# Optimization experiments

Hardware: AMD Instinct MI355X
Metric: run time of the kernel (lower is better)

Reference implementation:

```python
import jax, jax.numpy as jnp
import numpy as np

A, B, D, H = 64, 256, 128, 512  # seq rows, columns (encoder batch / decode loop), n_dims, hidden


def _lstm_step(Wih, Whh, bih, bhh, h, c, x):
    # x: [N, D], h/c: [N, H]; PyTorch gate order i, f, g, o
    gates = x @ Wih.T + bih + h @ Whh.T + bhh  # [N, 4H]
    i, f, g, o = jnp.split(gates, 4, axis=-1)
    c = jax.nn.sigmoid(f) * c + jax.nn.sigmoid(i) * jnp.tanh(g)
    h = jax.nn.sigmoid(o) * jnp.tanh(c)
    return h, c


def setup_inputs() -> dict:
    key = jax.random.key(0)
    ks = jax.random.split(key, 12)
    s = 0.05
    inp = {
        "input_tensor": jax.random.normal(ks[0], (A, B, D), jnp.float32),
        "enc_Wih": jax.random.normal(ks[1], (4 * H, D), jnp.float32) * s,
        "enc_Whh": jax.random.normal(ks[2], (4 * H, H), jnp.float32) * s,
        "enc_bih": jax.random.normal(ks[3], (4 * H,), jnp.float32) * s,
        "enc_bhh": jax.random.normal(ks[4], (4 * H,), jnp.float32) * s,
        "dec_Wih": jax.random.normal(ks[5], (4 * H, D), jnp.float32) * s,
        "dec_Whh": jax.random.normal(ks[6], (4 * H, H), jnp.float32) * s,
        "dec_bih": jax.random.normal(ks[7], (4 * H,), jnp.float32) * s,
        "dec_bhh": jax.random.normal(ks[8], (4 * H,), jnp.float32) * s,
        "lin_W": jax.random.normal(ks[9], (D, H), jnp.float32) * s,
        "lin_b": jax.random.normal(ks[10], (D,), jnp.float32) * s,
    }
    return inp


def reference(input_tensor, enc_Wih, enc_Whh, enc_bih, enc_bhh,
              dec_Wih, dec_Whh, dec_bih, dec_bhh, lin_W, lin_b):
    a, b, d = input_tensor.shape
    h_dim = enc_Whh.shape[1]
    dt = input_tensor.dtype

    # ---- encoder: seq-first LSTM over dim0 (len a), batch = b ----
    def e_step(hc, x_t):
        h, c = hc
        h, c = _lstm_step(enc_Wih, enc_Whh, enc_bih, enc_bhh, h, c, x_t)
        return (h, c), None

    h0 = jnp.zeros((b, h_dim), dt)
    (hN, cN), _ = jax.lax.scan(e_step, (h0, h0), input_tensor)
    # hidden[0][:, -1].unsqueeze(1): keep only the LAST batch element -> [1, H]
    dh, dc = hN[-1:], cN[-1:]

    # ---- decoder: loop i = b-1 .. 0; emit linear(h) then run length-a LSTM on column i ----
    def col_step(hc, x_col):  # x_col: [a, d]
        h, c = hc
        out_i = (h @ lin_W.T + lin_b)[0]  # [d], emitted BEFORE processing the column

        def t_step(hc2, x_t):
            h2, c2 = hc2
            h2, c2 = _lstm_step(dec_Wih, dec_Whh, dec_bih, dec_bhh, h2, c2, x_t[None])
            return (h2, c2), None

        (h, c), _ = jax.lax.scan(t_step, (h, c), x_col)
        return (h, c), out_i

    x_cols = jnp.flip(jnp.transpose(input_tensor, (1, 0, 2)), 0)  # [b, a, d], reversed i
    _, outs = jax.lax.scan(col_step, (dh, dc), x_cols)  # [b, d] in reversed order
    outs = jnp.flip(outs, 0)
    # outputs[:, i, :] = [1, d] row broadcast across all a rows
    return jnp.broadcast_to(outs[None, :, :], (a, b, d))
```

## Files before the change

### kernel.cpp

```cpp
#include <hip/hip_runtime.h>
#include <math.h>

#define A_ 64
#define B_ 256
#define D_ 128
#define H_ 512
#define STEPS_ENC 64
#define STEPS_TOT (64 + 16384)
#define NWG 32

#define XCC_GETREG_IMM (20 | (31 << 11))

#define OFF_XT    0
#define N_XT      (A_*D_*B_)
#define OFF_HT0   (OFF_XT + N_XT)
#define OFF_HT1   (OFF_HT0 + H_*B_)
#define OFF_CT    (OFF_HT1 + H_*B_)
#define OFF_HTAP  (OFF_CT + H_*B_)
#define OFF_HB64  (OFF_HTAP + B_*H_)
#define OFF_CINIT (OFF_HB64 + 4*H_)
#define OFF_ELECT (OFF_CINIT + H_)

__device__ __forceinline__ float tanhfast(float x) {
  return 1.0f - 2.0f * __builtin_amdgcn_rcpf(__expf(2.0f * x) + 1.0f);
}

__device__ __forceinline__ unsigned long long load_nt(const unsigned long long* p) {
  unsigned long long v;
  asm volatile("global_load_dwordx2 %0, %1, off nt\n\ts_waitcnt vmcnt(0)"
               : "=&v"(v) : "v"(p) : "memory");
  return v;
}
__device__ __forceinline__ unsigned long long load_inv(const unsigned long long* p) {
  unsigned long long v;
  asm volatile("buffer_inv sc0\n\t"
               "global_load_dwordx2 %0, %1, off nt\n\ts_waitcnt vmcnt(0)"
               : "=&v"(v) : "v"(p) : "memory");
  return v;
}
__device__ __forceinline__ void store_nt(unsigned long long* p, unsigned long long v) {
  asm volatile("global_store_dwordx2 %0, %1, off nt" :: "v"(p), "v"(v) : "memory");
}

template<int CTRL>
__device__ __forceinline__ float dpp_ror_add(float x) {
  int y = __builtin_amdgcn_update_dpp(0, __float_as_int(x), CTRL, 0xF, 0xF, false);
  return x + __int_as_float(y);
}
__device__ __forceinline__ float row_allsum16(float x) {
  x = dpp_ror_add<0x128>(x);
  x = dpp_ror_add<0x124>(x);
  x = dpp_ror_add<0x122>(x);
  x = dpp_ror_add<0x121>(x);
  return x;
}

#define HSP 36
#define HS_N (16 * HSP)

__global__ void init0(float* __restrict__ ws) {
  unsigned long long* HB = (unsigned long long*)(ws + OFF_HB64);
  int* EL = (int*)(ws + OFF_ELECT);
  int j = threadIdx.x;
  HB[H_ + j] = 0ull;
  HB[j]      = 0xFFFFFFFF00000000ull;
  if (j < 8) EL[j] = 0;
  if (j == 8) EL[8] = -1;
}

template<int PHASE>
__device__ __forceinline__ void lstm_phase(
    const float* __restrict__ in0,
    const float* __restrict__ Wih, const float* __restrict__ Whh,
    const float* __restrict__ bih, const float* __restrict__ bhh,
    unsigned long long* __restrict__ HB, float* __restrict__ HTAP,
    float* hstage,
    int w, int v, int l, float& c,
    float actA, float actB, float actC)
{
  const int g = l >> 4;
  const int j = l & 15;
  const int u = (w << 4) + v;
  const int R = (g << 9) + u;

  float4 wh[8];
#pragma unroll
  for (int k = 0; k < 8; ++k)
    wh[k] = *(const float4*)&Whh[R * H_ + (j << 5) + (k << 2)];
  float4 wx0 = *(const float4*)&Wih[R * D_ + (j << 3)];
  float4 wx1 = *(const float4*)&Wih[R * D_ + (j << 3) + 4];
  const float bias = (j == 0) ? (bih[R] + bhh[R]) : 0.f;

  const int pe = (v << 5) + (l & 31);

  const int s0 = (PHASE == 0) ? 0 : STEPS_ENC;
  const int s1 = (PHASE == 0) ? STEPS_ENC : STEPS_TOT;

  for (int s = s0; s < s1; ++s) {
    const float* xp;
    if (PHASE == 0) {
      xp = in0 + (s * B_ + 255) * D_;
    } else {
      const int sd = s - STEPS_ENC;
      xp = in0 + ((sd & 63) * B_ + (255 - (sd >> 6))) * D_;
    }
    float4 x0 = *(const float4*)(xp + (j << 3));
    float4 x1 = *(const float4*)(xp + (j << 3) + 4);

    unsigned long long* slot = &HB[(((s + 1) & 1) << 9) + pe];
    unsigned long long pk;
    int spins = 0;
    for (;;) {
      pk = ((++spins & 63) == 0) ? load_inv(slot) : load_nt(slot);
      if (__all((unsigned)(pk >> 32) == (unsigned)s)) break;
    }
    float* hbuf = hstage + (s & 1) * HS_N;
    if (l < 32) hbuf[(v * HSP) + (l & 31)] = __uint_as_float((unsigned)pk);

    float acc = bias
              + wx0.x * x0.x + wx0.y * x0.y + wx0.z * x0.z + wx0.w * x0.w
              + wx1.x * x1.x + wx1.y * x1.y + wx1.z * x1.z + wx1.w * x1.w;

    __syncthreads();

    const float4* hp = (const float4*)&hbuf[j * HSP];
#pragma unroll
    for (int k = 0; k < 8; ++k) {
      float4 h4 = hp[k];
      acc += wh[k].x * h4.x + wh[k].y * h4.y + wh[k].z * h4.z + wh[k].w * h4.w;
    }

    float a = row_allsum16(acc);
    a = fmaf(actA, __builtin_amdgcn_rcpf(__expf(actB * a) + 1.0f), actC);
    float ai = __shfl(a, 0);
    float af = __shfl(a, 16);
    float ag = __shfl(a, 32);
    float ao = __shfl(a, 48);
    c = af * c + ai * ag;
    float hn = ao * tanhfast(c);
    if (l == 0) {
      if ((s & 63) == 63) {
        int q = s >> 6;
        if (q < 256) HTAP[q * H_ + u] = hn;
      }
      unsigned long long opk =
          ((unsigned long long)(unsigned)(s + 1) << 32) | __float_as_uint(hn);
      store_nt(&HB[((s & 1) << 9) + u], opk);
    }
  }
}

__global__ __launch_bounds__(1024) void fused(
    const float* __restrict__ in0,
    const float* __restrict__ eWih, const float* __restrict__ eWhh,
    const float* __restrict__ ebih, const float* __restrict__ ebhh,
    const float* __restrict__ dWih, const float* __restrict__ dWhh,
    const float* __restrict__ dbih, const float* __restrict__ dbhh,
    float* __restrict__ ws)
{
  unsigned long long* HB = (unsigned long long*)(ws + OFF_HB64);
  float* HTAP = ws + OFF_HTAP;

  __shared__ __align__(16) float hstage[2][HS_N];
  __shared__ int role;

  const int tid = threadIdx.x;

  if (tid == 0) {
    unsigned xcc = ((unsigned)__builtin_amdgcn_s_getreg(XCC_GETREG_IMM)) & 7u;
    int* EL = (int*)(ws + OFF_ELECT);
    int r = __hip_atomic_fetch_add(&EL[xcc], 1, __ATOMIC_RELAXED,
                                   __HIP_MEMORY_SCOPE_AGENT);
    int myrole = -1;
    if (r < NWG) {
      if (r == NWG - 1) {
        int exp = -1;
        __hip_atomic_compare_exchange_strong(&EL[8], &exp, (int)xcc,
            __ATOMIC_RELAXED, __ATOMIC_RELAXED, __HIP_MEMORY_SCOPE_AGENT);
      }
      int wx;
      do {
        wx = __hip_atomic_load(&EL[8], __ATOMIC_RELAXED, __HIP_MEMORY_SCOPE_AGENT);
        if (wx == -1) __builtin_amdgcn_s_sleep(2);
      } while (wx == -1);
      if (wx == (int)xcc) myrole = r;
    }
    role = myrole;
  }
  __syncthreads();
  if (role < 0) return;
  const int w = role;

  const int v = tid >> 6;
  const int l = tid & 63;

  const int gate = l >> 4;
  const float actA = (gate == 2) ? -2.0f :  1.0f;
  const float actB = (gate == 2) ?  2.0f : -1.0f;
  const float actC = (gate == 2) ?  1.0f :  0.0f;

  float c = 0.f;

  lstm_phase<0>(in0, eWih, eWhh, ebih, ebhh, HB, HTAP, &hstage[0][0],
                w, v, l, c, actA, actB, actC);
  lstm_phase<1>(in0, dWih, dWhh, dbih, dbhh, HB, HTAP, &hstage[0][0],
                w, v, l, c, actA, actB, actC);
}

__global__ __launch_bounds__(128) void out_proj(
    const float* __restrict__ ws, const float* __restrict__ linW,
    const float* __restrict__ linb, float* __restrict__ out) {
  const float* HTAP = ws + OFF_HTAP;
  __shared__ float hs[H_];
  const int b = blockIdx.x;
  const int i = 255 - b;
  const int d = threadIdx.x;
  *(float4*)&hs[4 * d] = *(const float4*)&HTAP[i * H_ + 4 * d];
  __syncthreads();
  float acc = linb[d];
#pragma unroll 8
  for (int k = 0; k < H_; k += 4) {
    float4 w4 = *(const float4*)&linW[d * H_ + k];
    acc += w4.x * hs[k] + w4.y * hs[k + 1] + w4.z * hs[k + 2] + w4.w * hs[k + 3];
  }
  for (int a = 0; a < A_; ++a)
    out[(a * B_ + b) * D_ + d] = acc;
}

extern "C" void kernel_launch(void* const* d_in, const int* in_sizes, int n_in,
                              void* d_out, int out_size, void* d_ws, size_t ws_size,
                              hipStream_t stream) {
  const float* in0  = (const float*)d_in[0];
  const float* eWih = (const float*)d_in[1];
  const float* eWhh = (const float*)d_in[2];
  const float* ebih = (const float*)d_in[3];
  const float* ebhh = (const float*)d_in[4];
  const float* dWih = (const float*)d_in[5];
  const float* dWhh = (const float*)d_in[6];
  const float* dbih = (const float*)d_in[7];
  const float* dbhh = (const float*)d_in[8];
  const float* linW = (const float*)d_in[9];
  const float* linb = (const float*)d_in[10];
  float* ws = (float*)d_ws;
  float* out = (float*)d_out;

  init0<<<1, 512, 0, stream>>>(ws);
  fused<<<256, 1024, 0, stream>>>(in0, eWih, eWhh, ebih, ebhh,
                                  dWih, dWhh, dbih, dbhh, ws);
  out_proj<<<256, 128, 0, stream>>>(ws, linW, linb, out);
}
```

Measured before the change: 18.61 ms.

## Halve compute waves, use LDS counter barrier and dedicated publisher wave

Each compute wave now handles two hidden units using 8-lane groups per gate (16 float4 weights per lane), so 8 compute waves replace 16. The per-step __syncthreads is replaced by an LDS atomic counter barrier. A separate ninth wave takes over publishing the h values to global memory and the HTAP taps, so the compute waves only write to LDS. The aim is to cut per-step barrier and global-store latency on the serial recurrence, at the cost of higher register pressure and a custom spin barrier.

```diff
diff --git a/kernel.cpp b/kernel.cpp
--- a/kernel.cpp
+++ b/kernel.cpp
@@ -8,6 +8,8 @@
 #define STEPS_ENC 64
 #define STEPS_TOT (64 + 16384)
 #define NWG 32
+#define WAVES_C 8
+#define NTHREADS 576
 
 #define XCC_GETREG_IMM (20 | (31 << 11))
 
@@ -43,20 +45,19 @@
 }
 
 template<int CTRL>
-__device__ __forceinline__ float dpp_ror_add(float x) {
+__device__ __forceinline__ float dpp_add(float x) {
   int y = __builtin_amdgcn_update_dpp(0, __float_as_int(x), CTRL, 0xF, 0xF, false);
   return x + __int_as_float(y);
 }
-__device__ __forceinline__ float row_allsum16(float x) {
-  x = dpp_ror_add<0x128>(x);
-  x = dpp_ror_add<0x124>(x);
-  x = dpp_ror_add<0x122>(x);
-  x = dpp_ror_add<0x121>(x);
+__device__ __forceinline__ float grp8_allsum(float x) {
+  x = dpp_add<0x141>(x);
+  x = dpp_add<0x4E>(x);
+  x = dpp_add<0xB1>(x);
   return x;
 }
 
-#define HSP 36
-#define HS_N (16 * HSP)
+#define HSP 68
+#define HS_N 544
 
 __global__ void init0(float* __restrict__ ws) {
   unsigned long long* HB = (unsigned long long*)(ws + OFF_HB64);
@@ -73,25 +74,26 @@
     const float* __restrict__ in0,
     const float* __restrict__ Wih, const float* __restrict__ Whh,
     const float* __restrict__ bih, const float* __restrict__ bhh,
-    unsigned long long* __restrict__ HB, float* __restrict__ HTAP,
-    float* hstage,
-    int w, int v, int l, float& c,
+    unsigned long long* __restrict__ HB,
+    float (*hstage)[HS_N], unsigned long long* hout, unsigned int* cnt,
+    int w, int v, int l, float& c0, float& c1,
     float actA, float actB, float actC)
 {
-  const int g = l >> 4;
-  const int j = l & 15;
-  const int u = (w << 4) + v;
+  const int j = l & 7;
+  const int g = (l >> 3) & 3;
+  const int n = l >> 5;
+  const int u = (w << 4) + (v << 1) + n;
   const int R = (g << 9) + u;
 
-  float4 wh[8];
+  float4 wh[16];
 #pragma unroll
-  for (int k = 0; k < 8; ++k)
-    wh[k] = *(const float4*)&Whh[R * H_ + (j << 5) + (k << 2)];
-  float4 wx0 = *(const float4*)&Wih[R * D_ + (j << 3)];
-  float4 wx1 = *(const float4*)&Wih[R * D_ + (j << 3) + 4];
+  for (int k = 0; k < 16; ++k)
+    wh[k] = *(const float4*)&Whh[R * H_ + (j << 6) + (k << 2)];
+  float4 wx[4];
+#pragma unroll
+  for (int k = 0; k < 4; ++k)
+    wx[k] = *(const float4*)&Wih[R * D_ + (j << 4) + (k << 2)];
   const float bias = (j == 0) ? (bih[R] + bhh[R]) : 0.f;
-
-  const int pe = (v << 5) + (l & 31);
 
   const int s0 = (PHASE == 0) ? 0 : STEPS_ENC;
   const int s1 = (PHASE == 0) ? STEPS_ENC : STEPS_TOT;
@@ -104,53 +106,62 @@
       const int sd = s - STEPS_ENC;
       xp = in0 + ((sd & 63) * B_ + (255 - (sd >> 6))) * D_;
     }
-    float4 x0 = *(const float4*)(xp + (j << 3));
-    float4 x1 = *(const float4*)(xp + (j << 3) + 4);
-
-    unsigned long long* slot = &HB[(((s + 1) & 1) << 9) + pe];
+    float4 x0 = *(const float4*)(xp + (j << 4));
+    float4 x1 = *(const float4*)(xp + (j << 4) + 4);
+    float4 x2 = *(const float4*)(xp + (j << 4) + 8);
+    float4 x3 = *(const float4*)(xp + (j << 4) + 12);
+
+    unsigned long long* slot = &HB[(((s + 1) & 1) << 9) + (v << 6) + l];
     unsigned long long pk;
     int spins = 0;
     for (;;) {
       pk = ((++spins & 63) == 0) ? load_inv(slot) : load_nt(slot);
       if (__all((unsigned)(pk >> 32) == (unsigned)s)) break;
     }
-    float* hbuf = hstage + (s & 1) * HS_N;
-    if (l < 32) hbuf[(v * HSP) + (l & 31)] = __uint_as_float((unsigned)pk);
+    float* hbuf = hstage[s & 1];
+    hbuf[v * HSP + l] = __uint_as_float((unsigned)pk);
 
     float acc = bias
-              + wx0.x * x0.x + wx0.y * x0.y + wx0.z * x0.z + wx0.w * x0.w
-              + wx1.x * x1.x + wx1.y * x1.y + wx1.z * x1.z + wx1.w * x1.w;
-
-    __syncthreads();
+              + wx[0].x * x0.x + wx[0].y * x0.y + wx[0].z * x0.z + wx[0].w * x0.w
+              + wx[1].x * x1.x + wx[1].y * x1.y + wx[1].z * x1.z + wx[1].w * x1.w
+              + wx[2].x * x2.x + wx[2].y * x2.y + wx[2].z * x2.z + wx[2].w * x2.w
+              + wx[3].x * x3.x + wx[3].y * x3.y + wx[3].z * x3.z + wx[3].w * x3.w;
+
+    if (l == 0)
+      __hip_atomic_fetch_add(&cnt[s & 1], 1u, __ATOMIC_RELEASE,
+                             __HIP_MEMORY_SCOPE_WORKGROUP);
+    const unsigned target = 8u * ((unsigned)(s >> 1) + 1u);
+    while (__hip_atomic_load(&cnt[s & 1], __ATOMIC_ACQUIRE,
+                             __HIP_MEMORY_SCOPE_WORKGROUP) < target) {}
 
     const float4* hp = (const float4*)&hbuf[j * HSP];
 #pragma unroll
-    for (int k = 0; k < 8; ++k) {
+    for (int k = 0; k < 16; ++k) {
       float4 h4 = hp[k];
       acc += wh[k].x * h4.x + wh[k].y * h4.y + wh[k].z * h4.z + wh[k].w * h4.w;
     }
 
-    float a = row_allsum16(acc);
+    float a = grp8_allsum(acc);
     a = fmaf(actA, __builtin_amdgcn_rcpf(__expf(actB * a) + 1.0f), actC);
-    float ai = __shfl(a, 0);
-    float af = __shfl(a, 16);
-    float ag = __shfl(a, 32);
-    float ao = __shfl(a, 48);
-    c = af * c + ai * ag;
-    float hn = ao * tanhfast(c);
+    float ai0 = __shfl(a, 0),  af0 = __shfl(a, 8);
+    float ag0 = __shfl(a, 16), ao0 = __shfl(a, 24);
+    float ai1 = __shfl(a, 32), af1 = __shfl(a, 40);
+    float ag1 = __shfl(a, 48), ao1 = __shfl(a, 56);
+    c0 = af0 * c0 + ai0 * ag0;
+    c1 = af1 * c1 + ai1 * ag1;
+    float hn0 = ao0 * tanhfast(c0);
+    float hn1 = ao1 * tanhfast(c1);
     if (l == 0) {
-      if ((s & 63) == 63) {
-        int q = s >> 6;
-        if (q < 256) HTAP[q * H_ + u] = hn;
-      }
-      unsigned long long opk =
-          ((unsigned long long)(unsigned)(s + 1) << 32) | __float_as_uint(hn);
-      store_nt(&HB[((s & 1) << 9) + u], opk);
-    }
-  }
-}
-
-__global__ __launch_bounds__(1024) void fused(
+      const unsigned long long t = ((unsigned long long)(unsigned)(s + 1) << 32);
+      __hip_atomic_store(&hout[(v << 1)],     t | __float_as_uint(hn0),
+                         __ATOMIC_RELAXED, __HIP_MEMORY_SCOPE_WORKGROUP);
+      __hip_atomic_store(&hout[(v << 1) + 1], t | __float_as_uint(hn1),
+                         __ATOMIC_RELAXED, __HIP_MEMORY_SCOPE_WORKGROUP);
+    }
+  }
+}
+
+__global__ __launch_bounds__(NTHREADS) void fused(
     const float* __restrict__ in0,
     const float* __restrict__ eWih, const float* __restrict__ eWhh,
     const float* __restrict__ ebih, const float* __restrict__ ebhh,
@@ -162,9 +173,14 @@
   float* HTAP = ws + OFF_HTAP;
 
   __shared__ __align__(16) float hstage[2][HS_N];
+  __shared__ unsigned long long hout[16];
+  __shared__ unsigned int cnt[2];
   __shared__ int role;
 
   const int tid = threadIdx.x;
+
+  if (tid < 16) hout[tid] = 0xFFFFFFFF00000000ull;
+  if (tid < 2)  cnt[tid] = 0u;
 
   if (tid == 0) {
     unsigned xcc = ((unsigned)__builtin_amdgcn_s_getreg(XCC_GETREG_IMM)) & 7u;
@@ -191,20 +207,44 @@
   if (role < 0) return;
   const int w = role;
 
-  const int v = tid >> 6;
+  const int wid = tid >> 6;
   const int l = tid & 63;
 
-  const int gate = l >> 4;
+  if (wid == WAVES_C) {
+    const int u = (w << 4) + (l & 15);
+    for (int s = 0; s < STEPS_TOT; ++s) {
+      unsigned long long pk;
+      for (;;) {
+        pk = (l < 16)
+           ? __hip_atomic_load(&hout[l & 15], __ATOMIC_ACQUIRE,
+                               __HIP_MEMORY_SCOPE_WORKGROUP)
+           : (((unsigned long long)(unsigned)(s + 1)) << 32);
+        if (__all((unsigned)(pk >> 32) == (unsigned)(s + 1))) break;
+      }
+      if (l < 16) {
+        if ((s & 63) == 63) {
+          int q = s >> 6;
+          if (q < 256) HTAP[q * H_ + u] = __uint_as_float((unsigned)pk);
+        }
+        store_nt(&HB[((s & 1) << 9) + u], pk);
+      }
+    }
+    return;
+  }
+
+  const int v = wid;
+
+  const int gate = (l >> 3) & 3;
   const float actA = (gate == 2) ? -2.0f :  1.0f;
   const float actB = (gate == 2) ?  2.0f : -1.0f;
   const float actC = (gate == 2) ?  1.0f :  0.0f;
 
-  float c = 0.f;
-
-  lstm_phase<0>(in0, eWih, eWhh, ebih, ebhh, HB, HTAP, &hstage[0][0],
-                w, v, l, c, actA, actB, actC);
-  lstm_phase<1>(in0, dWih, dWhh, dbih, dbhh, HB, HTAP, &hstage[0][0],
-                w, v, l, c, actA, actB, actC);
+  float c0 = 0.f, c1 = 0.f;
+
+  lstm_phase<0>(in0, eWih, eWhh, ebih, ebhh, HB, hstage, hout, cnt,
+                w, v, l, c0, c1, actA, actB, actC);
+  lstm_phase<1>(in0, dWih, dWhh, dbih, dbhh, HB, hstage, hout, cnt,
+                w, v, l, c0, c1, actA, actB, actC);
 }
 
 __global__ __launch_bounds__(128) void out_proj(
@@ -245,7 +285,7 @@
   float* out = (float*)d_out;
 
   init0<<<1, 512, 0, stream>>>(ws);
-  fused<<<256, 1024, 0, stream>>>(in0, eWih, eWhh, ebih, ebhh,
-                                  dWih, dWhh, dbih, dbhh, ws);
+  fused<<<256, NTHREADS, 0, stream>>>(in0, eWih, eWhh, ebih, ebhh,
+                                      dWih, dWhh, dbih, dbhh, ws);
   out_proj<<<256, 128, 0, stream>>>(ws, linW, linb, out);
 }
```

Result: slower. 24.74 ms (+32.9%).

## Replace per-step workgroup barrier with LDS counter and prefetch next input

Applied to the files above, without the earlier changes.

Replaces the per-step __syncthreads with a monotonically increasing LDS counter per stage buffer. Each wave signals arrival and spins until all 16 waves have staged their h values. The input x for the next step is loaded one step ahead so its global latency overlaps the poll and compute. The recurrent dot product is split into two accumulators for more ILP. The cost is LDS atomic spinning in place of the hardware barrier.

```diff
diff --git a/kernel.cpp b/kernel.cpp
--- a/kernel.cpp
+++ b/kernel.cpp
@@ -8,6 +8,7 @@
 #define STEPS_ENC 64
 #define STEPS_TOT (64 + 16384)
 #define NWG 32
+#define NTHREADS 1024
 
 #define XCC_GETREG_IMM (20 | (31 << 11))
 
@@ -58,6 +59,12 @@
 #define HSP 36
 #define HS_N (16 * HSP)
 
+__device__ __forceinline__ const float* xaddr(const float* in0, int s) {
+  if (s < STEPS_ENC) return in0 + (s * B_ + 255) * D_;
+  int sd = s - STEPS_ENC;
+  return in0 + ((sd & 63) * B_ + (255 - (sd >> 6))) * D_;
+}
+
 __global__ void init0(float* __restrict__ ws) {
   unsigned long long* HB = (unsigned long long*)(ws + OFF_HB64);
   int* EL = (int*)(ws + OFF_ELECT);
@@ -74,8 +81,8 @@
     const float* __restrict__ Wih, const float* __restrict__ Whh,
     const float* __restrict__ bih, const float* __restrict__ bhh,
     unsigned long long* __restrict__ HB, float* __restrict__ HTAP,
-    float* hstage,
-    int w, int v, int l, float& c,
+    float (*hstage)[HS_N], unsigned int* cnt,
+    int w, int v, int l, float& c, float4 (&xc)[2],
     float actA, float actB, float actC)
 {
   const int g = l >> 4;
@@ -97,16 +104,6 @@
   const int s1 = (PHASE == 0) ? STEPS_ENC : STEPS_TOT;
 
   for (int s = s0; s < s1; ++s) {
-    const float* xp;
-    if (PHASE == 0) {
-      xp = in0 + (s * B_ + 255) * D_;
-    } else {
-      const int sd = s - STEPS_ENC;
-      xp = in0 + ((sd & 63) * B_ + (255 - (sd >> 6))) * D_;
-    }
-    float4 x0 = *(const float4*)(xp + (j << 3));
-    float4 x1 = *(const float4*)(xp + (j << 3) + 4);
-
     unsigned long long* slot = &HB[(((s + 1) & 1) << 9) + pe];
     unsigned long long pk;
     int spins = 0;
@@ -114,23 +111,41 @@
       pk = ((++spins & 63) == 0) ? load_inv(slot) : load_nt(slot);
       if (__all((unsigned)(pk >> 32) == (unsigned)s)) break;
     }
-    float* hbuf = hstage + (s & 1) * HS_N;
-    if (l < 32) hbuf[(v * HSP) + (l & 31)] = __uint_as_float((unsigned)pk);
-
-    float acc = bias
-              + wx0.x * x0.x + wx0.y * x0.y + wx0.z * x0.z + wx0.w * x0.w
-              + wx1.x * x1.x + wx1.y * x1.y + wx1.z * x1.z + wx1.w * x1.w;
-
-    __syncthreads();
+    float* hbuf = hstage[s & 1];
+    if (l < 32) hbuf[v * HSP + (l & 31)] = __uint_as_float((unsigned)pk);
+
+    if (l == 0)
+      __hip_atomic_fetch_add(&cnt[s & 1], 1u, __ATOMIC_RELEASE,
+                             __HIP_MEMORY_SCOPE_WORKGROUP);
+
+    float acc0 = bias
+               + wx0.x * xc[0].x + wx0.y * xc[0].y
+               + wx0.z * xc[0].z + wx0.w * xc[0].w
+               + wx1.x * xc[1].x + wx1.y * xc[1].y
+               + wx1.z * xc[1].z + wx1.w * xc[1].w;
+
+    int sn = s + 1; if (sn >= STEPS_TOT) sn = STEPS_TOT - 1;
+    const float* xp = xaddr(in0, sn);
+    float4 xn0 = *(const float4*)(xp + (j << 3));
+    float4 xn1 = *(const float4*)(xp + (j << 3) + 4);
+
+    const unsigned target = 16u * ((unsigned)(s >> 1) + 1u);
+    while (__hip_atomic_load(&cnt[s & 1], __ATOMIC_ACQUIRE,
+                             __HIP_MEMORY_SCOPE_WORKGROUP) < target) {}
 
     const float4* hp = (const float4*)&hbuf[j * HSP];
+    float acc1 = 0.f;
 #pragma unroll
-    for (int k = 0; k < 8; ++k) {
-      float4 h4 = hp[k];
-      acc += wh[k].x * h4.x + wh[k].y * h4.y + wh[k].z * h4.z + wh[k].w * h4.w;
-    }
-
-    float a = row_allsum16(acc);
+    for (int k = 0; k < 8; k += 2) {
+      float4 h4a = hp[k];
+      float4 h4b = hp[k + 1];
+      acc0 += wh[k].x * h4a.x + wh[k].y * h4a.y
+            + wh[k].z * h4a.z + wh[k].w * h4a.w;
+      acc1 += wh[k + 1].x * h4b.x + wh[k + 1].y * h4b.y
+            + wh[k + 1].z * h4b.z + wh[k + 1].w * h4b.w;
+    }
+
+    float a = row_allsum16(acc0 + acc1);
     a = fmaf(actA, __builtin_amdgcn_rcpf(__expf(actB * a) + 1.0f), actC);
     float ai = __shfl(a, 0);
     float af = __shfl(a, 16);
@@ -147,10 +162,11 @@
           ((unsigned long long)(unsigned)(s + 1) << 32) | __float_as_uint(hn);
       store_nt(&HB[((s & 1) << 9) + u], opk);
     }
-  }
-}
-
-__global__ __launch_bounds__(1024) void fused(
+    xc[0] = xn0; xc[1] = xn1;
+  }
+}
+
+__global__ __launch_bounds__(NTHREADS) void fused(
     const float* __restrict__ in0,
     const float* __restrict__ eWih, const float* __restrict__ eWhh,
     const float* __restrict__ ebih, const float* __restrict__ ebhh,
@@ -162,9 +178,12 @@
   float* HTAP = ws + OFF_HTAP;
 
   __shared__ __align__(16) float hstage[2][HS_N];
+  __shared__ unsigned int cnt[2];
   __shared__ int role;
 
   const int tid = threadIdx.x;
+
+  if (tid < 2) cnt[tid] = 0u;
 
   if (tid == 0) {
     unsigned xcc = ((unsigned)__builtin_amdgcn_s_getreg(XCC_GETREG_IMM)) & 7u;
@@ -201,10 +220,18 @@
 
   float c = 0.f;
 
-  lstm_phase<0>(in0, eWih, eWhh, ebih, ebhh, HB, HTAP, &hstage[0][0],
-                w, v, l, c, actA, actB, actC);
-  lstm_phase<1>(in0, dWih, dWhh, dbih, dbhh, HB, HTAP, &hstage[0][0],
-                w, v, l, c, actA, actB, actC);
+  float4 xc[2];
+  {
+    const int j = l & 15;
+    const float* xp = xaddr(in0, 0);
+    xc[0] = *(const float4*)(xp + (j << 3));
+    xc[1] = *(const float4*)(xp + (j << 3) + 4);
+  }
+
+  lstm_phase<0>(in0, eWih, eWhh, ebih, ebhh, HB, HTAP, hstage, cnt,
+                w, v, l, c, xc, actA, actB, actC);
+  lstm_phase<1>(in0, dWih, dWhh, dbih, dbhh, HB, HTAP, hstage, cnt,
+                w, v, l, c, xc, actA, actB, actC);
 }
 
 __global__ __launch_bounds__(128) void out_proj(
@@ -245,7 +272,7 @@
   float* out = (float*)d_out;
 
   init0<<<1, 512, 0, stream>>>(ws);
-  fused<<<256, 1024, 0, stream>>>(in0, eWih, eWhh, ebih, ebhh,
-                                  dWih, dWhh, dbih, dbhh, ws);
+  fused<<<256, NTHREADS, 0, stream>>>(in0, eWih, eWhh, ebih, ebhh,
+                                      dWih, dWhh, dbih, dbhh, ws);
   out_proj<<<256, 128, 0, stream>>>(ws, linW, linb, out);
 }
```

After: 18.98 ms. +2.0%, slower.
